# Performance work log

Measured on AMD Instinct MI355X. Metric: run time of the kernel, lower is better.

Reference implementation:

```python
import jax, jax.numpy as jnp
import numpy as np

D_HEAD = 64


def setup_inputs() -> dict:
    key = jax.random.key(0)
    ks = jax.random.split(key, 9)
    B, S, D, H, Dh = 2, 2048, 1024, 16, D_HEAD
    scale = 0.02
    return {
        "normalized_resid_pre": jax.random.normal(ks[0], (B, S, D), jnp.float32),
        "W_Q": jax.random.normal(ks[1], (H, D, Dh), jnp.float32) * scale,
        "W_K": jax.random.normal(ks[2], (H, D, Dh), jnp.float32) * scale,
        "W_V": jax.random.normal(ks[3], (H, D, Dh), jnp.float32) * scale,
        "W_O": jax.random.normal(ks[4], (H, Dh, D), jnp.float32) * scale,
        "b_Q": jax.random.normal(ks[5], (H, Dh), jnp.float32) * scale,
        "b_K": jax.random.normal(ks[6], (H, Dh), jnp.float32) * scale,
        "b_V": jax.random.normal(ks[7], (H, Dh), jnp.float32) * scale,
        "b_O": jax.random.normal(ks[8], (D,), jnp.float32) * scale,
    }


def reference(normalized_resid_pre, W_Q, W_K, W_V, W_O, b_Q, b_K, b_V, b_O):
    x = normalized_resid_pre  # [b, s, d]
    IGNORE = jnp.float32(-1e5)
    q = jnp.einsum('bsd,hde->bshe', x, W_Q) + b_Q  # [b, s, h, dh]
    k = jnp.einsum('bsd,hde->bshe', x, W_K) + b_K
    v = jnp.einsum('bsd,hde->bshe', x, W_V) + b_V
    scores = jnp.einsum('bqhe,bkhe->bhqk', q, k) / jnp.sqrt(jnp.float32(D_HEAD))
    S = scores.shape[-1]
    causal = jnp.tril(jnp.ones((S, S), dtype=bool))  # True where allowed
    scores = jnp.where(causal, scores, IGNORE)
    pattern = jax.nn.softmax(scores, axis=-1)
    z = jnp.einsum('bkhe,bhqk->bqhe', v, pattern)
    attn_out = jnp.einsum('bqhe,hed->bqd', z, W_O) + b_O
    return attn_out
```

## Files before the change

kernel.cpp:

```cpp
#include <hip/hip_runtime.h>

typedef float f32x4 __attribute__((ext_vector_type(4)));
typedef __bf16 bf16x8_t __attribute__((ext_vector_type(8)));
typedef __bf16 bf16x4_t __attribute__((ext_vector_type(4)));
typedef unsigned int u32x2 __attribute__((ext_vector_type(2)));

#define GLOAD16(gptr, lptr)                                                        \
  __builtin_amdgcn_global_load_lds((const __attribute__((address_space(1))) void*)(gptr), \
                                   (__attribute__((address_space(3))) void*)(lptr), 16, 0, 0)

__device__ inline float fexp2(float x) {
  float r;
  asm("v_exp_f32 %0, %1" : "=v"(r) : "v"(x));
  return r;
}

union VFu { bf16x8_t v8; u32x2 w[2]; };

#define TRR(d, B, OFF) \
  asm volatile("ds_read_b64_tr_b16 %0, %1 offset:" OFF : "=v"(d) : "v"(B))

__global__ __launch_bounds__(256) void k_prep(const float* __restrict__ x,
                                              const float* __restrict__ wq,
                                              const float* __restrict__ wk,
                                              const float* __restrict__ wv,
                                              const float* __restrict__ wo,
                                              const float* __restrict__ bq,
                                              const float* __restrict__ bk,
                                              const float* __restrict__ bv,
                                              __bf16* __restrict__ xb,
                                              __bf16* __restrict__ wb1,
                                              __bf16* __restrict__ wb2,
                                              float* __restrict__ b1) {
  __shared__ __bf16 tr[64][64];
  int bid = blockIdx.x, t = threadIdx.x;
  if (bid < 4096) {
    int i = bid * 256 + t;
    float4 a = reinterpret_cast<const float4*>(x)[i];
    bf16x4_t o;
    o[0] = (__bf16)a.x; o[1] = (__bf16)a.y; o[2] = (__bf16)a.z; o[3] = (__bf16)a.w;
    reinterpret_cast<bf16x4_t*>(xb)[i] = o;
  } else if (bid < 4864) {
    int k = bid - 4096;
    int dt = k & 15, h = (k >> 4) & 15, p = k >> 8;
    const float* W = (p == 0) ? wq : (p == 1) ? wk : wv;
#pragma unroll
    for (int i = 0; i < 4; ++i) {
      int fl = i * 1024 + t * 4;
      int dd = fl >> 6, e = fl & 63;
      float4 a = *reinterpret_cast<const float4*>(W + ((size_t)(h * 1024 + dt * 64 + dd) * 64 + e));
      tr[e + 0][dd] = (__bf16)a.x; tr[e + 1][dd] = (__bf16)a.y;
      tr[e + 2][dd] = (__bf16)a.z; tr[e + 3][dd] = (__bf16)a.w;
    }
    __syncthreads();
#pragma unroll
    for (int i = 0; i < 2; ++i) {
      int ch = i * 256 + t;
      int e = ch >> 3, c8 = ch & 7;
      *reinterpret_cast<bf16x8_t*>(wb1 + ((size_t)(p * 1024 + h * 64 + e) * 1024 + dt * 64 + c8 * 8)) =
          *reinterpret_cast<const bf16x8_t*>(&tr[e][c8 * 8]);
    }
  } else if (bid < 5120) {
    int k = bid - 4864;
    int nt = k & 15, h = k >> 4;
#pragma unroll
    for (int i = 0; i < 4; ++i) {
      int fl = i * 1024 + t * 4;
      int e = fl >> 6, nn = fl & 63;
      float4 a = *reinterpret_cast<const float4*>(wo + ((size_t)(h * 64 + e) * 1024 + nt * 64 + nn));
      tr[nn + 0][e] = (__bf16)a.x; tr[nn + 1][e] = (__bf16)a.y;
      tr[nn + 2][e] = (__bf16)a.z; tr[nn + 3][e] = (__bf16)a.w;
    }
    __syncthreads();
#pragma unroll
    for (int i = 0; i < 2; ++i) {
      int ch = i * 256 + t;
      int nn = ch >> 3, c8 = ch & 7;
      *reinterpret_cast<bf16x8_t*>(wb2 + ((size_t)(nt * 64 + nn) * 1024 + h * 64 + c8 * 8)) =
          *reinterpret_cast<const bf16x8_t*>(&tr[nn][c8 * 8]);
    }
  } else {
    int n = (bid - 5120) * 256 + t;
    if (n < 3072) {
      int p = n >> 10, he = n & 1023;
      const float* s = (p == 0) ? bq : (p == 1) ? bk : bv;
      b1[n] = s[he];
    }
  }
}

template <typename OutT, int MODE, int MT, int NT>
__global__ __launch_bounds__(256) void k_gemm(const __bf16* __restrict__ A,
                                              const __bf16* __restrict__ Bt,
                                              const float* __restrict__ bias,
                                              OutT* __restrict__ C, int N, int K) {
  __shared__ __bf16 As[MT * 64];
  __shared__ __bf16 Bs[NT * 64];
  constexpr int MI = MT / 32;
  constexpr int NR = NT / 32;
  constexpr int AI = MT / 32;
  constexpr int BI = NT / 32;
  int t = threadIdx.x, l = t & 63;
  int lo = l & 15, hi = l >> 4;
  int w = t >> 6;
  int bid = blockIdx.x;
  int xcd = bid & 7, loc = bid >> 3;
  int xc = N / NT;
  int rx = (int)gridDim.x / (8 * xc);
  int yy = loc / xc;
  int xx = loc - yy * xc;
  int m0 = (xcd * rx + yy) * MT, n0 = xx * NT;
  int wm = (w >> 1) * (MT / 2), wn = (w & 1) * (NT / 2);
  f32x4 acc[MI][NR] = {};
  for (int k0 = 0; k0 < K; k0 += 64) {
    __syncthreads();
#pragma unroll
    for (int it = 0; it < AI; ++it) {
      int idx = it * 256 + t;
      int row = idx >> 3, c = idx & 7;
      int cs = (c ^ (row & 7)) * 8;
      GLOAD16(A + (size_t)(m0 + row) * K + k0 + cs, (char*)As + (it * 256 + (t & ~63)) * 16);
    }
#pragma unroll
    for (int it = 0; it < BI; ++it) {
      int idx = it * 256 + t;
      int row = idx >> 3, c = idx & 7;
      int cs = (c ^ (row & 7)) * 8;
      GLOAD16(Bt + (size_t)(n0 + row) * K + k0 + cs, (char*)Bs + (it * 256 + (t & ~63)) * 16);
    }
    __syncthreads();
#pragma unroll
    for (int kc = 0; kc < 2; ++kc) {
      bf16x8_t af[MI], bfr[NR];
#pragma unroll
      for (int mi = 0; mi < MI; ++mi) {
        int row = wm + mi * 16 + lo;
        af[mi] = *reinterpret_cast<const bf16x8_t*>(
            (char*)As + row * 128 + (((kc * 4 + hi) ^ (row & 7)) << 4));
      }
#pragma unroll
      for (int ni = 0; ni < NR; ++ni) {
        int row = wn + ni * 16 + lo;
        bfr[ni] = *reinterpret_cast<const bf16x8_t*>(
            (char*)Bs + row * 128 + (((kc * 4 + hi) ^ (row & 7)) << 4));
      }
#pragma unroll
      for (int mi = 0; mi < MI; ++mi)
#pragma unroll
        for (int ni = 0; ni < NR; ++ni)
          acc[mi][ni] = __builtin_amdgcn_mfma_f32_16x16x32_bf16(af[mi], bfr[ni], acc[mi][ni], 0, 0, 0);
    }
  }
  float qs = (MODE == 1 && n0 < 1024) ? 0.18033688f : 1.0f;
#pragma unroll
  for (int ni = 0; ni < NR; ++ni) {
    int n = n0 + wn + ni * 16 + lo;
    float bv = bias[n];
    int p = n >> 10, hh = (n >> 6) & 15, e = n & 63;
#pragma unroll
    for (int mi = 0; mi < MI; ++mi) {
#pragma unroll
      for (int r = 0; r < 4; ++r) {
        int m = m0 + wm + mi * 16 + hi * 4 + r;
        if (MODE == 0) {
          C[(size_t)m * N + n] = (OutT)(acc[mi][ni][r] + bv);
        } else {
          int b = m >> 11, sr = m & 2047;
          C[(size_t)(p * 32 + b * 16 + hh) * 131072 + sr * 64 + e] =
              (OutT)((acc[mi][ni][r] + bv) * qs);
        }
      }
    }
  }
}

__global__ __launch_bounds__(256, 4) void k_attn(const __bf16* __restrict__ QKVh,
                                                 __bf16* __restrict__ Z) {
  __shared__ __bf16 Ks[2][64 * 64];
  __shared__ __bf16 Vs[2][64 * 64];
  __shared__ __bf16 Ps[64 * 64];
  int t = threadIdx.x, l = t & 63, w = t >> 6;
  int lo = l & 15, hi = l >> 4;
  int bid = blockIdx.x;
  int xcd = bid & 7, kk = bid >> 3;
  int i = kk & 31, bhl = kk >> 5;
  int bh = xcd * 4 + bhl;
  int b = bh >> 4, h = bh & 15;
  int s16 = (w >> 1) * 64 + ((w & 1) ? (63 - i) : i);
  int qbase = s16 * 16;
  int ntW = (s16 >> 2) + 1;
  int ntH = ((127 - i) >> 2) + 1;

  const __bf16* Qbase = QKVh + (size_t)bh * 131072;
  const __bf16* Kbase = QKVh + (size_t)(32 + bh) * 131072;
  const __bf16* Vbase = QKVh + (size_t)(64 + bh) * 131072;

  int kSrc[2], vSrc[2];
#pragma unroll
  for (int it = 0; it < 2; ++it) {
    int idx = it * 256 + t;
    int row = idx >> 3, c = idx & 7;
    kSrc[it] = row * 64 + ((c ^ (row & 7)) * 8);
    int kv = ((idx >> 1) & 3) | (((idx >> 5) & 1) << 2) | (((idx >> 3) & 3) << 3) |
             (((idx >> 8) & 1) << 5);
    int e0s = ((idx & 1) << 3) | (((idx >> 6) & 3) << 4);
    vSrc[it] = kv * 64 + e0s;
  }

  bf16x8_t qf[2];
  {
    const __bf16* qptr = Qbase + (qbase + lo) * 64;
    qf[0] = *reinterpret_cast<const bf16x8_t*>(qptr + hi * 8);
    qf[1] = *reinterpret_cast<const bf16x8_t*>(qptr + 32 + hi * 8);
  }

  f32x4 zacc[4] = {};
  float lsum = 0.f;
  float mrow = -1e30f;

#define STAGE_KV(buf, tile)                                                             \
  {                                                                                     \
    GLOAD16(Kbase + (tile) * 4096 + kSrc[0], (char*)Ks[buf] + (t & ~63) * 16);          \
    GLOAD16(Kbase + (tile) * 4096 + kSrc[1], (char*)Ks[buf] + 4096 + (t & ~63) * 16);   \
    GLOAD16(Vbase + (tile) * 4096 + vSrc[0], (char*)Vs[buf] + (t & ~63) * 16);          \
    GLOAD16(Vbase + (tile) * 4096 + vSrc[1], (char*)Vs[buf] + 4096 + (t & ~63) * 16);   \
  }

  STAGE_KV(0, 0);
  __syncthreads();

  for (int tile = 0; tile < ntH; ++tile) {
    int cur = tile & 1, kv0 = tile * 64;
    bool havenext = (tile + 1 < ntH);
    if (havenext) {
      STAGE_KV(cur ^ 1, tile + 1);
      __builtin_amdgcn_sched_barrier(0);
    }
    if (tile < ntW) {
      f32x4 s[4] = {};
      __builtin_amdgcn_s_setprio(1);
#pragma unroll
      for (int cb = 0; cb < 4; ++cb) {
        int krow = cb * 16 + lo;
        const char* kp = (const char*)Ks[cur] + krow * 128;
        bf16x8_t kf0 = *reinterpret_cast<const bf16x8_t*>(kp + ((hi ^ (krow & 7)) << 4));
        bf16x8_t kf1 = *reinterpret_cast<const bf16x8_t*>(kp + (((4 + hi) ^ (krow & 7)) << 4));
        s[cb] = __builtin_amdgcn_mfma_f32_16x16x32_bf16(kf0, qf[0], s[cb], 0, 0, 0);
        s[cb] = __builtin_amdgcn_mfma_f32_16x16x32_bf16(kf1, qf[1], s[cb], 0, 0, 0);
      }
      __builtin_amdgcn_s_setprio(0);
      {
        int qabs = qbase + lo;
        if (tile == ntW - 1) {
#pragma unroll
          for (int cb = 0; cb < 4; ++cb)
#pragma unroll
            for (int r = 0; r < 4; ++r)
              if (kv0 + cb * 16 + hi * 4 + r > qabs) s[cb][r] = -1e30f;
        }
        float mt = -1e30f;
#pragma unroll
        for (int cb = 0; cb < 4; ++cb) {
          float m01 = fmaxf(s[cb][0], s[cb][1]);
          float m23 = fmaxf(s[cb][2], s[cb][3]);
          mt = fmaxf(mt, fmaxf(m01, m23));
        }
        mt = fmaxf(mt, __shfl_xor(mt, 16));
        mt = fmaxf(mt, __shfl_xor(mt, 32));
        if (!__all(mt - mrow <= 8.0f)) {
          float mnew = fmaxf(mrow, mt);
          float alpha = fexp2(mrow - mnew);
          mrow = mnew;
          lsum *= alpha;
#pragma unroll
          for (int r = 0; r < 4; ++r) {
            float at = __shfl(alpha, hi * 4 + r);
#pragma unroll
            for (int e0 = 0; e0 < 4; ++e0) zacc[e0][r] *= at;
          }
        }
        float psum = 0.f;
        int prow = w * 16 + lo;
        char* prp = (char*)Ps + prow * 128 + (hi & 1) * 8;
        int rsw = prow & 7;
#pragma unroll
        for (int cb = 0; cb < 4; ++cb) {
          bf16x4_t pp;
#pragma unroll
          for (int r = 0; r < 4; ++r) {
            float p = fexp2(s[cb][r] - mrow);
            psum += p;
            pp[r] = (__bf16)p;
          }
          *reinterpret_cast<bf16x4_t*>(prp + (((cb * 2 + (hi >> 1)) ^ rsw) << 4)) = pp;
        }
        lsum += psum;
      }
      __builtin_amdgcn_s_setprio(1);
      {
        const __attribute__((address_space(3))) char* vb =
            (const __attribute__((address_space(3))) char*)((char*)Vs[cur]) + l * 8;
        int arow = w * 16 + lo;
        char* psb = (char*)Ps + arow * 128;
        const __attribute__((address_space(3))) char* pp0 =
            (const __attribute__((address_space(3))) char*)(psb + ((hi ^ (arow & 7)) << 4));
        const __attribute__((address_space(3))) char* pp1 =
            (const __attribute__((address_space(3))) char*)(psb + (((4 + hi) ^ (arow & 7)) << 4));
        bf16x8_t pf0, pf1;
        asm volatile("ds_read_b128 %0, %1" : "=v"(pf0) : "v"(pp0) : "memory");
        asm volatile("ds_read_b128 %0, %1" : "=v"(pf1) : "v"(pp1) : "memory");
        VFu u[8];
        TRR(u[0].w[0], vb, "0");    TRR(u[0].w[1], vb, "512");
        TRR(u[1].w[0], vb, "1024"); TRR(u[1].w[1], vb, "1536");
        TRR(u[2].w[0], vb, "2048"); TRR(u[2].w[1], vb, "2560");
        TRR(u[3].w[0], vb, "3072"); TRR(u[3].w[1], vb, "3584");
        TRR(u[4].w[0], vb, "4096"); TRR(u[4].w[1], vb, "4608");
        TRR(u[5].w[0], vb, "5120"); TRR(u[5].w[1], vb, "5632");
        TRR(u[6].w[0], vb, "6144"); TRR(u[6].w[1], vb, "6656");
        TRR(u[7].w[0], vb, "7168"); TRR(u[7].w[1], vb, "7680");
        asm volatile("s_waitcnt lgkmcnt(8)" ::: "memory");
        __builtin_amdgcn_sched_barrier(0);
        zacc[0] = __builtin_amdgcn_mfma_f32_16x16x32_bf16(pf0, u[0].v8, zacc[0], 0, 0, 0);
        zacc[1] = __builtin_amdgcn_mfma_f32_16x16x32_bf16(pf0, u[1].v8, zacc[1], 0, 0, 0);
        zacc[2] = __builtin_amdgcn_mfma_f32_16x16x32_bf16(pf0, u[2].v8, zacc[2], 0, 0, 0);
        zacc[3] = __builtin_amdgcn_mfma_f32_16x16x32_bf16(pf0, u[3].v8, zacc[3], 0, 0, 0);
        asm volatile("s_waitcnt lgkmcnt(0)" ::: "memory");
        __builtin_amdgcn_sched_barrier(0);
        zacc[0] = __builtin_amdgcn_mfma_f32_16x16x32_bf16(pf1, u[4].v8, zacc[0], 0, 0, 0);
        zacc[1] = __builtin_amdgcn_mfma_f32_16x16x32_bf16(pf1, u[5].v8, zacc[1], 0, 0, 0);
        zacc[2] = __builtin_amdgcn_mfma_f32_16x16x32_bf16(pf1, u[6].v8, zacc[2], 0, 0, 0);
        zacc[3] = __builtin_amdgcn_mfma_f32_16x16x32_bf16(pf1, u[7].v8, zacc[3], 0, 0, 0);
      }
      __builtin_amdgcn_s_setprio(0);
    }
    __syncthreads();
  }

  float lt = lsum;
  lt += __shfl_xor(lt, 16);
  lt += __shfl_xor(lt, 32);
  float inv = 1.0f / lt;
#pragma unroll
  for (int r = 0; r < 4; ++r) {
    float lv = __shfl(inv, hi * 4 + r);
    size_t row = (size_t)(b * 2048 + qbase + hi * 4 + r);
#pragma unroll
    for (int e0 = 0; e0 < 4; ++e0)
      Z[row * 1024 + h * 64 + e0 * 16 + lo] = (__bf16)(zacc[e0][r] * lv);
  }
#undef STAGE_KV
}


extern "C" void kernel_launch(void* const* d_in, const int* in_sizes, int n_in,
                              void* d_out, int out_size, void* d_ws, size_t ws_size,
                              hipStream_t stream) {
  const float* x  = (const float*)d_in[0];
  const float* wq = (const float*)d_in[1];
  const float* wk = (const float*)d_in[2];
  const float* wv = (const float*)d_in[3];
  const float* wo = (const float*)d_in[4];
  const float* bq = (const float*)d_in[5];
  const float* bk = (const float*)d_in[6];
  const float* bv = (const float*)d_in[7];
  const float* bo = (const float*)d_in[8];
  float* out = (float*)d_out;

  char* ws = (char*)d_ws;
  __bf16* Xb   = (__bf16*)(ws);
  __bf16* WB1  = (__bf16*)(ws + 8388608);
  float*  B1   = (float*)(ws + 14680064);
  __bf16* WB2  = (__bf16*)(ws + 14692352);
  __bf16* QKVh = (__bf16*)(ws + 16789504);
  __bf16* Zb   = Xb;

  k_prep<<<5132, 256, 0, stream>>>(x, wq, wk, wv, wo, bq, bk, bv, Xb, WB1, WB2, B1);
  k_gemm<__bf16, 1, 128, 128><<<768, 256, 0, stream>>>(Xb, WB1, B1, QKVh, 3072, 1024);
  k_attn<<<1024, 256, 0, stream>>>(QKVh, Zb);
  k_gemm<float, 0, 64, 64><<<1024, 256, 0, stream>>>(Zb, WB2, bo, out, 1024, 1024);
}
```

Baseline: 120.9 us.

## Load K fragments directly from global into registers instead of staging through LDS

Drops the shared-memory double buffer for K. Each wave now loads its K MFMA fragments straight from global memory into registers, and prefetches the next tile's fragments after the current QK^T MFMAs are issued. This removes LDS traffic and LDS capacity for K. In exchange it adds redundant global or L2 reads across the four waves and raises register pressure from the eight bf16x8 prefetch registers. Global-load latency may now be exposed before the next tile's MFMAs.

Measured after the change: 206.9 us. 1.71x slower.

```diff
diff --git a/kernel.cpp b/kernel.cpp
--- a/kernel.cpp
+++ b/kernel.cpp
@@ -176,7 +176,6 @@
 
 __global__ __launch_bounds__(256, 4) void k_attn(const __bf16* __restrict__ QKVh,
                                                  __bf16* __restrict__ Z) {
-  __shared__ __bf16 Ks[2][64 * 64];
   __shared__ __bf16 Vs[2][64 * 64];
   __shared__ __bf16 Ps[64 * 64];
   int t = threadIdx.x, l = t & 63, w = t >> 6;
@@ -195,17 +194,17 @@
   const __bf16* Kbase = QKVh + (size_t)(32 + bh) * 131072;
   const __bf16* Vbase = QKVh + (size_t)(64 + bh) * 131072;
 
-  int kSrc[2], vSrc[2];
+  int vSrc[2];
 #pragma unroll
   for (int it = 0; it < 2; ++it) {
     int idx = it * 256 + t;
-    int row = idx >> 3, c = idx & 7;
-    kSrc[it] = row * 64 + ((c ^ (row & 7)) * 8);
     int kv = ((idx >> 1) & 3) | (((idx >> 5) & 1) << 2) | (((idx >> 3) & 3) << 3) |
              (((idx >> 8) & 1) << 5);
     int e0s = ((idx & 1) << 3) | (((idx >> 6) & 3) << 4);
     vSrc[it] = kv * 64 + e0s;
   }
+
+  const __bf16* kp = Kbase + lo * 64 + hi * 8;
 
   bf16x8_t qf[2];
   {
@@ -217,38 +216,47 @@
   f32x4 zacc[4] = {};
   float lsum = 0.f;
   float mrow = -1e30f;
-
-#define STAGE_KV(buf, tile)                                                             \
+  bf16x8_t kf[8];
+
+#define LOAD_K(tile)                                                                    \
   {                                                                                     \
-    GLOAD16(Kbase + (tile) * 4096 + kSrc[0], (char*)Ks[buf] + (t & ~63) * 16);          \
-    GLOAD16(Kbase + (tile) * 4096 + kSrc[1], (char*)Ks[buf] + 4096 + (t & ~63) * 16);   \
+    const __bf16* kpt = kp + (size_t)(tile) * 4096;                                     \
+    _Pragma("unroll") for (int cb = 0; cb < 4; ++cb) {                                  \
+      kf[cb * 2]     = *reinterpret_cast<const bf16x8_t*>(kpt + cb * 1024);             \
+      kf[cb * 2 + 1] = *reinterpret_cast<const bf16x8_t*>(kpt + cb * 1024 + 32);        \
+    }                                                                                   \
+  }
+
+#define STAGE_V(buf, tile)                                                              \
+  {                                                                                     \
     GLOAD16(Vbase + (tile) * 4096 + vSrc[0], (char*)Vs[buf] + (t & ~63) * 16);          \
     GLOAD16(Vbase + (tile) * 4096 + vSrc[1], (char*)Vs[buf] + 4096 + (t & ~63) * 16);   \
   }
 
-  STAGE_KV(0, 0);
+  LOAD_K(0);
+  STAGE_V(0, 0);
   __syncthreads();
 
   for (int tile = 0; tile < ntH; ++tile) {
     int cur = tile & 1, kv0 = tile * 64;
     bool havenext = (tile + 1 < ntH);
+    bool active = (tile < ntW);
+    f32x4 s[4] = {};
+    if (active) {
+      __builtin_amdgcn_s_setprio(1);
+#pragma unroll
+      for (int cb = 0; cb < 4; ++cb) {
+        s[cb] = __builtin_amdgcn_mfma_f32_16x16x32_bf16(kf[cb * 2], qf[0], s[cb], 0, 0, 0);
+        s[cb] = __builtin_amdgcn_mfma_f32_16x16x32_bf16(kf[cb * 2 + 1], qf[1], s[cb], 0, 0, 0);
+      }
+      __builtin_amdgcn_s_setprio(0);
+    }
     if (havenext) {
-      STAGE_KV(cur ^ 1, tile + 1);
+      LOAD_K(tile + 1);
+      STAGE_V(cur ^ 1, tile + 1);
       __builtin_amdgcn_sched_barrier(0);
     }
-    if (tile < ntW) {
-      f32x4 s[4] = {};
-      __builtin_amdgcn_s_setprio(1);
-#pragma unroll
-      for (int cb = 0; cb < 4; ++cb) {
-        int krow = cb * 16 + lo;
-        const char* kp = (const char*)Ks[cur] + krow * 128;
-        bf16x8_t kf0 = *reinterpret_cast<const bf16x8_t*>(kp + ((hi ^ (krow & 7)) << 4));
-        bf16x8_t kf1 = *reinterpret_cast<const bf16x8_t*>(kp + (((4 + hi) ^ (krow & 7)) << 4));
-        s[cb] = __builtin_amdgcn_mfma_f32_16x16x32_bf16(kf0, qf[0], s[cb], 0, 0, 0);
-        s[cb] = __builtin_amdgcn_mfma_f32_16x16x32_bf16(kf1, qf[1], s[cb], 0, 0, 0);
-      }
-      __builtin_amdgcn_s_setprio(0);
+    if (active) {
       {
         int qabs = qbase + lo;
         if (tile == ntW - 1) {
@@ -348,7 +356,8 @@
     for (int e0 = 0; e0 < 4; ++e0)
       Z[row * 1024 + h * 64 + e0 * 16 + lo] = (__bf16)(zacc[e0][r] * lv);
   }
-#undef STAGE_KV
+#undef LOAD_K
+#undef STAGE_V
 }
 
 
```
